# Performance work log

Hardware: AMD Instinct MI355X
Metric: run time of the kernel (lower is better)

## Reference

```python
import jax, jax.numpy as jnp
import numpy as np
from jax import lax

EPS = 1e-5
NUM_HEADS = 8


def _safe_norm(x):
    # sqrt(max(sum x^2, EPS^2)) == max(||x||, EPS); grad-safe at 0
    return jnp.sqrt(jnp.maximum(jnp.sum(x * x, axis=-1, keepdims=True), EPS * EPS))


def _project(x):
    norm = _safe_norm(x)
    max_norm = 1.0 - EPS
    scale = jnp.where(norm >= max_norm, max_norm / (norm + EPS), jnp.ones_like(norm))
    return x * scale


def _logmap0(y):
    # logarithmic_map(0, y): lambda_0 = 2/(1+EPS)
    y = _project(y)
    n = _safe_norm(y)  # clamp(min=EPS) is built in
    lam = 2.0 / (1.0 + EPS)
    return (2.0 / lam) * jnp.arctanh(n) * (y / n)


def _expmap0(v):
    # exponential_map(0, v): lambda_0 = 2/(1+EPS)
    n = _safe_norm(v)
    lam = 2.0 / (1.0 + EPS)
    return _project(jnp.tanh(lam * n / 2.0) * (v / n))


def _mobius_add(x, y):
    x = _project(x)
    y = _project(y)
    xy = jnp.sum(x * y, axis=-1, keepdims=True)
    xn = jnp.sum(x * x, axis=-1, keepdims=True)
    yn = jnp.sum(y * y, axis=-1, keepdims=True)
    num = (1.0 + 2.0 * xy + yn) * x + (1.0 - xn) * y
    den = 1.0 + 2.0 * xy + xn * yn + EPS
    return _project(num / den)


def _hyp_linear(x, W, b):
    # HyperbolicLinear.forward: project -> logmap0 -> linear -> expmap0 -> mobius-add bias
    x = _project(x)
    xt = _logmap0(x)
    t = xt @ W.T
    r = _expmap0(t)
    r = _mobius_add(r, jnp.broadcast_to(b, r.shape))
    return r


def setup_inputs() -> dict:
    key = jax.random.key(0)
    ks = jax.random.split(key, 11)
    B, S, E = 4, 512, 512

    def xavier(k, shape):
        bound = np.sqrt(6.0 / (shape[0] + shape[1]))
        return jax.random.uniform(k, shape, jnp.float32, -bound, bound)

    return {
        "query": jax.random.normal(ks[0], (B, S, E), jnp.float32),
        "key": jax.random.normal(ks[1], (B, S, E), jnp.float32),
        "value": jax.random.normal(ks[2], (B, S, E), jnp.float32),
        "Wq": xavier(ks[3], (E, E)), "bq": 0.01 * jax.random.normal(ks[4], (E,), jnp.float32),
        "Wk": xavier(ks[5], (E, E)), "bk": 0.01 * jax.random.normal(ks[6], (E,), jnp.float32),
        "Wv": xavier(ks[7], (E, E)), "bv": 0.01 * jax.random.normal(ks[8], (E,), jnp.float32),
        "Wo": xavier(ks[9], (E, E)), "bo": 0.01 * jax.random.normal(ks[10], (E,), jnp.float32),
    }


def reference(query, key, value, Wq, bq, Wk, bk, Wv, bv, Wo, bo):
    B, S, E = query.shape
    H = NUM_HEADS
    D = E // H

    Q = _hyp_linear(query, Wq, bq).reshape(B, S, H, D).transpose(0, 2, 1, 3)  # [B,H,S,D]
    K = _hyp_linear(key, Wk, bk).reshape(B, S, H, D).transpose(0, 2, 1, 3)
    V = _hyp_linear(value, Wv, bv).reshape(B, S, H, D).transpose(0, 2, 1, 3)

    # Pairwise Poincare distance: d(q,k) = acosh(1 + 2||q-k||^2/((1-|q|^2)(1-|k|^2)) + EPS)
    q = _project(Q)
    k = _project(K)
    qn = jnp.sum(q * q, axis=-1)  # [B,H,S]
    kn = jnp.sum(k * k, axis=-1)  # [B,H,S]
    qk = jnp.einsum('bhqd,bhkd->bhqk', q, k)
    num = jnp.maximum(qn[..., :, None] + kn[..., None, :] - 2.0 * qk, 0.0)
    den = jnp.maximum((1.0 - qn)[..., :, None] * (1.0 - kn)[..., None, :], EPS)
    dist = jnp.arccosh(1.0 + 2.0 * num / den + EPS)  # [B,H,Sq,Sk]
    attn = jax.nn.softmax(-dist, axis=-1)

    # Sequential Mobius-add accumulation over key/value positions
    wt = jnp.moveaxis(attn, 3, 0)  # [Sk,B,H,Sq]
    vt = jnp.moveaxis(V, 2, 0)     # [Sk,B,H,D]

    @jax.checkpoint
    def step(ws, wv):
        wj, vj = wv  # wj: [B,H,Sq], vj: [B,H,D]
        return _mobius_add(ws, wj[..., None] * vj[:, :, None, :]), None

    ws0 = jnp.zeros((B, H, S, D), query.dtype)
    attended, _ = lax.scan(step, ws0, (wt, vt))  # [B,H,Sq,D]

    attended = attended.transpose(0, 2, 1, 3).reshape(B, S, E)
    return _hyp_linear(attended, Wo, bo)
```

## Files before the change

kernel.cpp:

```cpp
#include <hip/hip_runtime.h>
#include <math.h>

#define EPS  1e-5f
#define EPS2 1e-10f
#define MAXN (1.0f - EPS)

using short8  = __attribute__((ext_vector_type(8))) short;
using floatx4 = __attribute__((ext_vector_type(4))) float;
using float2v = __attribute__((ext_vector_type(2))) float;

template <int CTRL>
static __device__ __forceinline__ float qperm(float x) {
  return __int_as_float(__builtin_amdgcn_update_dpp(
      __float_as_int(x), __float_as_int(x), CTRL, 0xF, 0xF, false));
}
#define QP_XOR1    0xB1
#define QP_XOR2    0x4E
#define QP_HALFMIR 0x141

#if __has_builtin(__builtin_elementwise_fma)
static __device__ __forceinline__ float2v fma2(float2v a, float2v b, float2v c) {
  return __builtin_elementwise_fma(a, b, c);
}
#else
static __device__ __forceinline__ float2v fma2(float2v a, float2v b, float2v c) {
  float2v r; r.x = fmaf(a.x, b.x, c.x); r.y = fmaf(a.y, b.y, c.y); return r;
}
#endif

static __device__ __forceinline__ int pack_hi2(float a, float b) {
  return (int)((__float_as_uint(a) >> 16) | (__float_as_uint(b) & 0xFFFF0000u));
}
static __device__ __forceinline__ float hi_of(float a) {
  return __uint_as_float(__float_as_uint(a) & 0xFFFF0000u);
}

static __device__ __forceinline__ float logmap_f(float ss) {
  const float r = sqrtf(fmaxf(ss, EPS2));
  float at;
  if (r >= MAXN) {
    at = 0.5f * logf((r * (2.0f - EPS) + EPS) / (EPS * (1.0f + r)));
  } else {
    at = 0.5f * logf((1.0f + r) / (1.0f - r));
  }
  return (1.0f + EPS) * at / r;
}

__global__ __launch_bounds__(256) void k_gemm_mfma(
    const float* __restrict__ A0, const float* __restrict__ A1, const float* __restrict__ A2,
    const float* __restrict__ W0, const float* __restrict__ W1, const float* __restrict__ W2,
    float* __restrict__ Cbase) {
  const int z = blockIdx.z;
  const float* A = (z == 0) ? A0 : ((z == 1) ? A1 : A2);
  const float* W = (z == 0) ? W0 : ((z == 1) ? W1 : W2);
  float* C = Cbase + (size_t)z * (2048 * 512);
  __shared__ int Ahi[64][36], Alo[64][36], Whi[64][36], Wlo[64][36];
  __shared__ float f_lds[64];
  const int t = threadIdx.x;
  const int n0 = blockIdx.x * 64;
  const int m0 = blockIdx.y * 64;
  const int row = t >> 2, c0 = (t & 3) * 16, ci = (t & 3) * 8;
  const int w = t >> 6, lane = t & 63;
  const int quad = lane >> 4, l16 = lane & 15;
  const int mw = (w & 1) * 32, nw = (w >> 1) * 32;
  floatx4 acc[2][2];
#pragma unroll
  for (int i = 0; i < 2; ++i)
#pragma unroll
    for (int j = 0; j < 2; ++j) acc[i][j] = (floatx4){0.f, 0.f, 0.f, 0.f};
  float ssq = 0.0f;

  for (int k0 = 0; k0 < 512; k0 += 64) {
    float4 av[4], wv[4];
#pragma unroll
    for (int i = 0; i < 4; ++i) {
      av[i] = *(const float4*)&A[(size_t)(n0 + row) * 512 + k0 + c0 + 4 * i];
      wv[i] = *(const float4*)&W[(size_t)(m0 + row) * 512 + k0 + c0 + 4 * i];
    }
    int pAh[8], pAl[8], pWh[8], pWl[8];
#pragma unroll
    for (int i = 0; i < 4; ++i) {
      ssq = fmaf(av[i].x, av[i].x, ssq); ssq = fmaf(av[i].y, av[i].y, ssq);
      ssq = fmaf(av[i].z, av[i].z, ssq); ssq = fmaf(av[i].w, av[i].w, ssq);
      pAh[2 * i]     = pack_hi2(av[i].x, av[i].y);
      pAh[2 * i + 1] = pack_hi2(av[i].z, av[i].w);
      pAl[2 * i]     = pack_hi2(av[i].x - hi_of(av[i].x), av[i].y - hi_of(av[i].y));
      pAl[2 * i + 1] = pack_hi2(av[i].z - hi_of(av[i].z), av[i].w - hi_of(av[i].w));
      pWh[2 * i]     = pack_hi2(wv[i].x, wv[i].y);
      pWh[2 * i + 1] = pack_hi2(wv[i].z, wv[i].w);
      pWl[2 * i]     = pack_hi2(wv[i].x - hi_of(wv[i].x), wv[i].y - hi_of(wv[i].y));
      pWl[2 * i + 1] = pack_hi2(wv[i].z - hi_of(wv[i].z), wv[i].w - hi_of(wv[i].w));
    }
    __syncthreads();
    *(int4*)&Ahi[row][ci]     = *(int4*)&pAh[0];
    *(int4*)&Ahi[row][ci + 4] = *(int4*)&pAh[4];
    *(int4*)&Alo[row][ci]     = *(int4*)&pAl[0];
    *(int4*)&Alo[row][ci + 4] = *(int4*)&pAl[4];
    *(int4*)&Whi[row][ci]     = *(int4*)&pWh[0];
    *(int4*)&Whi[row][ci + 4] = *(int4*)&pWh[4];
    *(int4*)&Wlo[row][ci]     = *(int4*)&pWl[0];
    *(int4*)&Wlo[row][ci + 4] = *(int4*)&pWl[4];
    __syncthreads();
#pragma unroll
    for (int kk = 0; kk < 64; kk += 32) {
      short8 ah[2], al[2], bh[2], bl[2];
#pragma unroll
      for (int i = 0; i < 2; ++i) {
        ah[i] = *(const short8*)&((const short*)Ahi[mw + i * 16 + l16])[kk + quad * 8];
        al[i] = *(const short8*)&((const short*)Alo[mw + i * 16 + l16])[kk + quad * 8];
        bh[i] = *(const short8*)&((const short*)Whi[nw + i * 16 + l16])[kk + quad * 8];
        bl[i] = *(const short8*)&((const short*)Wlo[nw + i * 16 + l16])[kk + quad * 8];
      }
#pragma unroll
      for (int i = 0; i < 2; ++i)
#pragma unroll
        for (int j = 0; j < 2; ++j) {
          acc[i][j] = __builtin_amdgcn_mfma_f32_16x16x32_bf16(ah[i], bh[j], acc[i][j], 0, 0, 0);
          acc[i][j] = __builtin_amdgcn_mfma_f32_16x16x32_bf16(ah[i], bl[j], acc[i][j], 0, 0, 0);
          acc[i][j] = __builtin_amdgcn_mfma_f32_16x16x32_bf16(al[i], bh[j], acc[i][j], 0, 0, 0);
        }
    }
  }
  ssq += qperm<QP_XOR1>(ssq);
  ssq += qperm<QP_XOR2>(ssq);
  if ((t & 3) == 0) f_lds[row] = logmap_f(ssq);
  __syncthreads();
#pragma unroll
  for (int i = 0; i < 2; ++i) {
    const int lrow_base = mw + i * 16 + quad * 4;
#pragma unroll
    for (int r = 0; r < 4; ++r) {
      const float fv = f_lds[lrow_base + r];
#pragma unroll
      for (int j = 0; j < 2; ++j)
        C[(size_t)(n0 + lrow_base + r) * 512 + m0 + nw + j * 16 + l16] = fv * acc[i][j][r];
    }
  }
}

__global__ __launch_bounds__(256) void k_post(const float* __restrict__ tin,
                                              const float* __restrict__ b0,
                                              const float* __restrict__ b1,
                                              const float* __restrict__ b2,
                                              float* __restrict__ o0, float* __restrict__ o1,
                                              float* __restrict__ o2,
                                              float* __restrict__ nrm0, float* __restrict__ nrm1,
                                              float* __restrict__ nrm2,
                                              float* __restrict__ rowsum_init, int final_mode) {
  const int nrow = blockIdx.x, z = blockIdx.y, t = threadIdx.x;
  const float* tv = tin + ((size_t)z * 2048 + nrow) * 512;
  const float* bias = (z == 0) ? b0 : ((z == 1) ? b1 : b2);
  const int e0 = 2 * t;
  const float2 tp = *(const float2*)&tv[e0];
  const float2 bp = *(const float2*)&bias[e0];
  float p_tt = tp.x * tp.x + tp.y * tp.y;
  float p_tb = tp.x * bp.x + tp.y * bp.y;
  float p_bb = bp.x * bp.x + bp.y * bp.y;
#pragma unroll
  for (int m = 32; m; m >>= 1) {
    p_tt += __shfl_xor(p_tt, m, 64);
    p_tb += __shfl_xor(p_tb, m, 64);
    p_bb += __shfl_xor(p_bb, m, 64);
  }
  __shared__ float red[4][3];
  const int lane = t & 63, w = t >> 6;
  if (lane == 0) { red[w][0] = p_tt; red[w][1] = p_tb; red[w][2] = p_bb; }
  __syncthreads();
  const float s_tt = red[0][0] + red[1][0] + red[2][0] + red[3][0];
  const float s_tb = red[0][1] + red[1][1] + red[2][1] + red[3][1];
  const float s_bb = red[0][2] + red[1][2] + red[2][2] + red[3][2];
  const float tn = sqrtf(fmaxf(s_tt, EPS2));
  const float th = tanhf(tn / (1.0f + EPS));
  const float g = th / tn;
  const float rnorm = th * (sqrtf(s_tt) / tn);
  const float sr = (rnorm >= MAXN) ? (MAXN / (rnorm + EPS)) : 1.0f;
  const float gr = g * sr;
  const float rn = (rnorm * sr) * (rnorm * sr);
  const float bnorm = sqrtf(fmaxf(s_bb, EPS2));
  const float sb = (bnorm >= MAXN) ? (MAXN / (bnorm + EPS)) : 1.0f;
  const float xy = gr * sb * s_tb;
  const float yn = (sb * sb) * s_bb;
  const float Af = 1.0f + 2.0f * xy + yn;
  const float Cf = 1.0f - rn;
  const float den = 1.0f + 2.0f * xy + rn * yn + EPS;
  const float id = 1.0f / den;
  const float on_raw = (Af * Af * rn + 2.0f * Af * Cf * xy + Cf * Cf * yn) * (id * id);
  const float no = sqrtf(fmaxf(on_raw, EPS2));
  const float so = (no >= MAXN) ? (MAXN / (no + EPS)) : 1.0f;
  const float ms = id * so;
  const float ca = gr * Af * ms;
  const float cb = sb * Cf * ms;
  const float v0 = ca * tp.x + cb * bp.x;
  const float v1 = ca * tp.y + cb * bp.y;
  if (final_mode) {
    float2 o; o.x = v0; o.y = v1;
    *(float2*)&o0[(size_t)nrow * 512 + e0] = o;
    return;
  }
  float hp = v0 * v0 + v1 * v1;
#pragma unroll
  for (int m = 16; m; m >>= 1) hp += __shfl_xor(hp, m, 64);
  const float hnr = sqrtf(fmaxf(hp, EPS2));
  float sh = 1.0f;
  if (z != 2) sh = (hnr >= MAXN) ? (MAXN / (hnr + EPS)) : 1.0f;
  float* outz = (z == 0) ? o0 : ((z == 1) ? o1 : o2);
  float* nz = (z == 0) ? nrm0 : ((z == 1) ? nrm1 : nrm2);
  const int b = nrow >> 9, s = nrow & 511, h = e0 >> 6, d = e0 & 63;
  float2 o; o.x = v0 * sh; o.y = v1 * sh;
  *(float2*)&outz[(((size_t)(b * 8 + h) * 512 + s) * 64 + d)] = o;
  if ((t & 31) == 0) nz[(size_t)(b * 8 + h) * 512 + s] = hp * sh * sh;
  if (z == 0 && t < 8) rowsum_init[((size_t)(nrow >> 9) * 8 + t) * 512 + (nrow & 511)] = 0.0f;
}

__global__ __launch_bounds__(256) void k_logits(const float* __restrict__ Q,
                                                const float* __restrict__ K,
                                                const float* __restrict__ qn,
                                                const float* __restrict__ kn,
                                                float* __restrict__ attn,
                                                float* __restrict__ rowsum) {
  const int bh = blockIdx.z;
  const int i0 = blockIdx.x * 64;
  const int j0 = blockIdx.y * 64;
  const float* Qb = Q + (size_t)bh * 512 * 64;
  const float* Kb = K + (size_t)bh * 512 * 64;
  __shared__ int Qhi[64][36], Qlo[64][36], Khi[64][36], Klo[64][36];
  const int t = threadIdx.x;
  const int row = t >> 2, c0 = (t & 3) * 16, ci = (t & 3) * 8;
  const int w = t >> 6, lane = t & 63;
  const int quad = lane >> 4, l16 = lane & 15;
  const int mw = (w & 1) * 32, nw = (w >> 1) * 32;
  float4 qv4[4], kv4[4];
#pragma unroll
  for (int i = 0; i < 4; ++i) {
    qv4[i] = *(const float4*)&Qb[(size_t)(i0 + row) * 64 + c0 + 4 * i];
    kv4[i] = *(const float4*)&Kb[(size_t)(j0 + row) * 64 + c0 + 4 * i];
  }
  int pQh[8], pQl[8], pKh[8], pKl[8];
#pragma unroll
  for (int i = 0; i < 4; ++i) {
    pQh[2 * i]     = pack_hi2(qv4[i].x, qv4[i].y);
    pQh[2 * i + 1] = pack_hi2(qv4[i].z, qv4[i].w);
    pQl[2 * i]     = pack_hi2(qv4[i].x - hi_of(qv4[i].x), qv4[i].y - hi_of(qv4[i].y));
    pQl[2 * i + 1] = pack_hi2(qv4[i].z - hi_of(qv4[i].z), qv4[i].w - hi_of(qv4[i].w));
    pKh[2 * i]     = pack_hi2(kv4[i].x, kv4[i].y);
    pKh[2 * i + 1] = pack_hi2(kv4[i].z, kv4[i].w);
    pKl[2 * i]     = pack_hi2(kv4[i].x - hi_of(kv4[i].x), kv4[i].y - hi_of(kv4[i].y));
    pKl[2 * i + 1] = pack_hi2(kv4[i].z - hi_of(kv4[i].z), kv4[i].w - hi_of(kv4[i].w));
  }
  *(int4*)&Qhi[row][ci]     = *(int4*)&pQh[0];
  *(int4*)&Qhi[row][ci + 4] = *(int4*)&pQh[4];
  *(int4*)&Qlo[row][ci]     = *(int4*)&pQl[0];
  *(int4*)&Qlo[row][ci + 4] = *(int4*)&pQl[4];
  *(int4*)&Khi[row][ci]     = *(int4*)&pKh[0];
  *(int4*)&Khi[row][ci + 4] = *(int4*)&pKh[4];
  *(int4*)&Klo[row][ci]     = *(int4*)&pKl[0];
  *(int4*)&Klo[row][ci + 4] = *(int4*)&pKl[4];
  __syncthreads();
  floatx4 acc[2][2];
#pragma unroll
  for (int i = 0; i < 2; ++i)
#pragma unroll
    for (int j = 0; j < 2; ++j) acc[i][j] = (floatx4){0.f, 0.f, 0.f, 0.f};
#pragma unroll
  for (int kk = 0; kk < 64; kk += 32) {
    short8 ah[2], al[2], bhv[2], blv[2];
#pragma unroll
    for (int i = 0; i < 2; ++i) {
      ah[i]  = *(const short8*)&((const short*)Qhi[mw + i * 16 + l16])[kk + quad * 8];
      al[i]  = *(const short8*)&((const short*)Qlo[mw + i * 16 + l16])[kk + quad * 8];
      bhv[i] = *(const short8*)&((const short*)Khi[nw + i * 16 + l16])[kk + quad * 8];
      blv[i] = *(const short8*)&((const short*)Klo[nw + i * 16 + l16])[kk + quad * 8];
    }
#pragma unroll
    for (int i = 0; i < 2; ++i)
#pragma unroll
      for (int j = 0; j < 2; ++j) {
        acc[i][j] = __builtin_amdgcn_mfma_f32_16x16x32_bf16(ah[i], bhv[j], acc[i][j], 0, 0, 0);
        acc[i][j] = __builtin_amdgcn_mfma_f32_16x16x32_bf16(ah[i], blv[j], acc[i][j], 0, 0, 0);
        acc[i][j] = __builtin_amdgcn_mfma_f32_16x16x32_bf16(al[i], bhv[j], acc[i][j], 0, 0, 0);
      }
  }
#pragma unroll
  for (int i = 0; i < 2; ++i) {
    float rs_acc[4] = {0.f, 0.f, 0.f, 0.f};
#pragma unroll
    for (int r = 0; r < 4; ++r) {
      const int grow = i0 + mw + i * 16 + quad * 4 + r;
      const float qni = qn[(size_t)bh * 512 + grow];
      const float rq = 1.0f - qni;
#pragma unroll
      for (int j = 0; j < 2; ++j) {
        const int gcol = j0 + nw + j * 16 + l16;
        const float knj = kn[(size_t)bh * 512 + gcol];
        const float num = fmaxf(qni + knj - 2.0f * acc[i][j][r], 0.0f);
        const float den = fmaxf(rq * (1.0f - knj), EPS);
        const float wv = fmaf(2.0f * num, __builtin_amdgcn_rcpf(den), EPS);
        const float s_ = 1.0f + wv + sqrtf(wv * (wv + 2.0f));
        const float rr = __builtin_amdgcn_rcpf(s_);
        rs_acc[r] += rr;
        attn[((size_t)bh * 512 + grow) * 512 + gcol] = rr;
      }
    }
#pragma unroll
    for (int r = 0; r < 4; ++r) {
      float v = rs_acc[r];
      v += __shfl_xor(v, 1, 64); v += __shfl_xor(v, 2, 64);
      v += __shfl_xor(v, 4, 64); v += __shfl_xor(v, 8, 64);
      if (l16 == 0)
        atomicAdd(&rowsum[(size_t)bh * 512 + i0 + mw + i * 16 + quad * 4 + r], v);
    }
  }
}

__global__ __launch_bounds__(256) void k_scan(const float* __restrict__ V,
                                              const float* __restrict__ vn,
                                              const float* __restrict__ rw,
                                              const float* __restrict__ rowsum,
                                              float* __restrict__ att) {
  __shared__ __align__(16) float v_lds[64 * 64];
  __shared__ __align__(16) float swyn_lds[64 * 66];
  const int blk = blockIdx.x;
  const int bh = blk >> 4;
  const int i0 = (blk & 15) * 32;
  const int t = threadIdx.x;
  const int lane = t & 63, w = t >> 6;
  const int row_blk = w * 8 + (lane >> 3);
  const int sub = lane & 7;
  const int d0 = sub * 8;
  const float* Vb = V + (size_t)bh * 512 * 64;
  const float* vnb = vn + (size_t)bh * 512;
  const float* arow = rw + ((size_t)bh * 512 + i0 + row_blk) * 512;
  const float inv_s = __builtin_amdgcn_rcpf(rowsum[(size_t)bh * 512 + i0 + row_blk]);

  float2v wsv[4];
#pragma unroll
  for (int k = 0; k < 4; ++k) wsv[k] = (float2v){0.f, 0.f};
  float xn = 0.0f;

  for (int jc = 0; jc < 512; jc += 64) {
#pragma unroll
    for (int it = 0; it < 4; ++it) {
      const int idx4 = it * 256 + t;
      *(float4*)&v_lds[idx4 * 4] = *(const float4*)&Vb[(size_t)jc * 64 + idx4 * 4];
    }
    const float4 a0 = *(const float4*)&arow[jc + sub * 8];
    const float4 a1 = *(const float4*)&arow[jc + sub * 8 + 4];
    const float4 n0 = *(const float4*)&vnb[jc + sub * 8];
    const float4 n1 = *(const float4*)&vnb[jc + sub * 8 + 4];
    const float wq[8] = {a0.x, a0.y, a0.z, a0.w, a1.x, a1.y, a1.z, a1.w};
    const float nq[8] = {n0.x, n0.y, n0.z, n0.w, n1.x, n1.y, n1.z, n1.w};
#pragma unroll
    for (int e = 0; e < 8; ++e) {
      const float wgt = wq[e] * inv_s;
      float2 p; p.x = wgt; p.y = (wgt * wgt) * nq[e];
      *(float2*)&swyn_lds[(sub * 8 + e) * 66 + row_blk * 2] = p;
    }
    __syncthreads();

#pragma unroll
    for (int j = 0; j < 64; ++j) {
      const float2 sy2 = *(const float2*)&swyn_lds[j * 66 + row_blk * 2];
      const float4 v0 = *(const float4*)&v_lds[j * 64 + d0];
      const float4 v1 = *(const float4*)&v_lds[j * 64 + d0 + 4];
      const float2v vv0 = {v0.x, v0.y}, vv1 = {v0.z, v0.w};
      const float2v vv2 = {v1.x, v1.y}, vv3 = {v1.z, v1.w};
      const float sw = sy2.x, yn = sy2.y;
      const float xnyn1 = fmaf(xn, yn, 1.0f + EPS);
      const float sxy   = xn + yn;
      const float ynp1  = 1.0f + yn;
      const float Cfsw  = (1.0f - xn) * sw;
      float2v da = wsv[0] * vv0;
      da = fma2(wsv[1], vv1, da);
      float2v db = wsv[2] * vv2;
      db = fma2(wsv[3], vv3, db);
      const float2v sv = da + db;
      float d = sv.x + sv.y;
      d += qperm<QP_XOR1>(d);
      d += qperm<QP_XOR2>(d);
      d += qperm<QP_HALFMIR>(d);
      const float xy  = sw * d;
      const float den = fmaf(2.0f, xy, xnyn1);
      const float s2  = fmaf(2.0f, xy, sxy);
      const float Af  = fmaf(2.0f, xy, ynp1);
      const float id  = __builtin_amdgcn_rcpf(den);
      const float dn  = den - EPS;
      const float am  = Af * id;
      const float cm  = Cfsw * id;
      xn = (s2 * id) * (dn * id);
      const float2v amv = {am, am};
      const float2v cmv = {cm, cm};
      wsv[0] = fma2(amv, wsv[0], cmv * vv0);
      wsv[1] = fma2(amv, wsv[1], cmv * vv1);
      wsv[2] = fma2(amv, wsv[2], cmv * vv2);
      wsv[3] = fma2(amv, wsv[3], cmv * vv3);
    }
    __syncthreads();
  }
  const int b = bh >> 3, h = bh & 7;
  float* o = att + (((size_t)b * 512 + i0 + row_blk) * 512 + h * 64 + d0);
  float4 s0; s0.x = wsv[0].x; s0.y = wsv[0].y; s0.z = wsv[1].x; s0.w = wsv[1].y;
  float4 s1; s1.x = wsv[2].x; s1.y = wsv[2].y; s1.z = wsv[3].x; s1.w = wsv[3].y;
  *(float4*)&o[0] = s0;
  *(float4*)&o[4] = s1;
}

extern "C" void kernel_launch(void* const* d_in, const int* in_sizes, int n_in,
                              void* d_out, int out_size, void* d_ws, size_t ws_size,
                              hipStream_t stream) {
  const float* query = (const float*)d_in[0];
  const float* key_  = (const float*)d_in[1];
  const float* value = (const float*)d_in[2];
  const float* Wq = (const float*)d_in[3];
  const float* bq = (const float*)d_in[4];
  const float* Wk = (const float*)d_in[5];
  const float* bk = (const float*)d_in[6];
  const float* Wv = (const float*)d_in[7];
  const float* bv = (const float*)d_in[8];
  const float* Wo = (const float*)d_in[9];
  const float* bo = (const float*)d_in[10];
  float* ws = (float*)d_ws;
  const size_t M = 1u << 20;
  float* Qb     = ws;
  float* Kb     = ws + 1 * M;
  float* Vb     = ws + 2 * M;
  float* qn     = ws + 3 * M;
  float* kn     = qn + 16384;
  float* vn     = kn + 16384;
  float* rowsum = vn + 16384;
  float* rw     = ws + 4 * M;
  float* t3     = ws + 12 * M;
  float* att    = ws + 15 * M;
  float* to_    = ws + 16 * M;

  k_gemm_mfma<<<dim3(32, 8, 3), 256, 0, stream>>>(query, key_, value, Wq, Wk, Wv, t3);
  k_post<<<dim3(2048, 3), 256, 0, stream>>>(t3, bq, bk, bv, Qb, Kb, Vb, qn, kn, vn,
                                            rowsum, 0);
  k_logits<<<dim3(8, 8, 32), 256, 0, stream>>>(Qb, Kb, qn, kn, rw, rowsum);
  k_scan<<<512, 256, 0, stream>>>(Vb, vn, rw, rowsum, att);
  k_gemm_mfma<<<dim3(32, 8, 1), 256, 0, stream>>>(att, att, att, Wo, Wo, Wo, to_);
  k_post<<<dim3(2048, 1), 256, 0, stream>>>(to_, bo, bo, bo, (float*)d_out,
                                            nullptr, nullptr, nullptr, nullptr, nullptr,
                                            nullptr, 1);
}
```

Before: 229.9 us.

## Split scan rows across 16 lanes with 4 dims each, doubling grid

The sequential Mobius-add scan kernel now gives each query row to 16 lanes holding 4 head dimensions each, instead of 8 lanes holding 8. Each block covers 16 rows, and the grid doubles to 1024 blocks. This shortens the per-lane serial dependency chain and raises the number of waves to hide latency on the sequential recurrence. In exchange it adds one more DPP reduction step per iteration, and each block reloads the V tile for half as many rows, doubling V traffic into LDS.

```diff
diff --git a/kernel.cpp b/kernel.cpp
--- a/kernel.cpp
+++ b/kernel.cpp
@@ -17,6 +17,7 @@
 #define QP_XOR1    0xB1
 #define QP_XOR2    0x4E
 #define QP_HALFMIR 0x141
+#define QP_MIRROR  0x140
 
 #if __has_builtin(__builtin_elementwise_fma)
 static __device__ __forceinline__ float2v fma2(float2v a, float2v b, float2v c) {
@@ -318,23 +319,20 @@
                                               const float* __restrict__ rowsum,
                                               float* __restrict__ att) {
   __shared__ __align__(16) float v_lds[64 * 64];
-  __shared__ __align__(16) float swyn_lds[64 * 66];
+  __shared__ __align__(16) float swyn_lds[64 * 34];
   const int blk = blockIdx.x;
-  const int bh = blk >> 4;
-  const int i0 = (blk & 15) * 32;
+  const int bh = blk >> 5;
+  const int i0 = (blk & 31) * 16;
   const int t = threadIdx.x;
-  const int lane = t & 63, w = t >> 6;
-  const int row_blk = w * 8 + (lane >> 3);
-  const int sub = lane & 7;
-  const int d0 = sub * 8;
+  const int row_blk = t >> 4;
+  const int sub = t & 15;
+  const int d0 = sub * 4;
   const float* Vb = V + (size_t)bh * 512 * 64;
   const float* vnb = vn + (size_t)bh * 512;
   const float* arow = rw + ((size_t)bh * 512 + i0 + row_blk) * 512;
   const float inv_s = __builtin_amdgcn_rcpf(rowsum[(size_t)bh * 512 + i0 + row_blk]);
 
-  float2v wsv[4];
-#pragma unroll
-  for (int k = 0; k < 4; ++k) wsv[k] = (float2v){0.f, 0.f};
+  float2v ws0 = {0.f, 0.f}, ws1 = {0.f, 0.f};
   float xn = 0.0f;
 
   for (int jc = 0; jc < 512; jc += 64) {
@@ -343,41 +341,35 @@
       const int idx4 = it * 256 + t;
       *(float4*)&v_lds[idx4 * 4] = *(const float4*)&Vb[(size_t)jc * 64 + idx4 * 4];
     }
-    const float4 a0 = *(const float4*)&arow[jc + sub * 8];
-    const float4 a1 = *(const float4*)&arow[jc + sub * 8 + 4];
-    const float4 n0 = *(const float4*)&vnb[jc + sub * 8];
-    const float4 n1 = *(const float4*)&vnb[jc + sub * 8 + 4];
-    const float wq[8] = {a0.x, a0.y, a0.z, a0.w, a1.x, a1.y, a1.z, a1.w};
-    const float nq[8] = {n0.x, n0.y, n0.z, n0.w, n1.x, n1.y, n1.z, n1.w};
-#pragma unroll
-    for (int e = 0; e < 8; ++e) {
+    const float4 aw = *(const float4*)&arow[jc + sub * 4];
+    const float4 nv = *(const float4*)&vnb[jc + sub * 4];
+    const float wq[4] = {aw.x, aw.y, aw.z, aw.w};
+    const float nq[4] = {nv.x, nv.y, nv.z, nv.w};
+#pragma unroll
+    for (int e = 0; e < 4; ++e) {
       const float wgt = wq[e] * inv_s;
       float2 p; p.x = wgt; p.y = (wgt * wgt) * nq[e];
-      *(float2*)&swyn_lds[(sub * 8 + e) * 66 + row_blk * 2] = p;
+      *(float2*)&swyn_lds[(sub * 4 + e) * 34 + row_blk * 2] = p;
     }
     __syncthreads();
 
 #pragma unroll
     for (int j = 0; j < 64; ++j) {
-      const float2 sy2 = *(const float2*)&swyn_lds[j * 66 + row_blk * 2];
-      const float4 v0 = *(const float4*)&v_lds[j * 64 + d0];
-      const float4 v1 = *(const float4*)&v_lds[j * 64 + d0 + 4];
-      const float2v vv0 = {v0.x, v0.y}, vv1 = {v0.z, v0.w};
-      const float2v vv2 = {v1.x, v1.y}, vv3 = {v1.z, v1.w};
+      const float2 sy2 = *(const float2*)&swyn_lds[j * 34 + row_blk * 2];
+      const float4 v4 = *(const float4*)&v_lds[j * 64 + d0];
+      const float2v vv0 = {v4.x, v4.y}, vv1 = {v4.z, v4.w};
       const float sw = sy2.x, yn = sy2.y;
       const float xnyn1 = fmaf(xn, yn, 1.0f + EPS);
       const float sxy   = xn + yn;
       const float ynp1  = 1.0f + yn;
       const float Cfsw  = (1.0f - xn) * sw;
-      float2v da = wsv[0] * vv0;
-      da = fma2(wsv[1], vv1, da);
-      float2v db = wsv[2] * vv2;
-      db = fma2(wsv[3], vv3, db);
-      const float2v sv = da + db;
-      float d = sv.x + sv.y;
+      float2v da = ws0 * vv0;
+      da = fma2(ws1, vv1, da);
+      float d = da.x + da.y;
       d += qperm<QP_XOR1>(d);
       d += qperm<QP_XOR2>(d);
       d += qperm<QP_HALFMIR>(d);
+      d += qperm<QP_MIRROR>(d);
       const float xy  = sw * d;
       const float den = fmaf(2.0f, xy, xnyn1);
       const float s2  = fmaf(2.0f, xy, sxy);
@@ -389,19 +381,15 @@
       xn = (s2 * id) * (dn * id);
       const float2v amv = {am, am};
       const float2v cmv = {cm, cm};
-      wsv[0] = fma2(amv, wsv[0], cmv * vv0);
-      wsv[1] = fma2(amv, wsv[1], cmv * vv1);
-      wsv[2] = fma2(amv, wsv[2], cmv * vv2);
-      wsv[3] = fma2(amv, wsv[3], cmv * vv3);
+      ws0 = fma2(amv, ws0, cmv * vv0);
+      ws1 = fma2(amv, ws1, cmv * vv1);
     }
     __syncthreads();
   }
   const int b = bh >> 3, h = bh & 7;
   float* o = att + (((size_t)b * 512 + i0 + row_blk) * 512 + h * 64 + d0);
-  float4 s0; s0.x = wsv[0].x; s0.y = wsv[0].y; s0.z = wsv[1].x; s0.w = wsv[1].y;
-  float4 s1; s1.x = wsv[2].x; s1.y = wsv[2].y; s1.z = wsv[3].x; s1.w = wsv[3].y;
+  float4 s0; s0.x = ws0.x; s0.y = ws0.y; s0.z = ws1.x; s0.w = ws1.y;
   *(float4*)&o[0] = s0;
-  *(float4*)&o[4] = s1;
 }
 
 extern "C" void kernel_launch(void* const* d_in, const int* in_sizes, int n_in,
@@ -436,7 +424,7 @@
   k_post<<<dim3(2048, 3), 256, 0, stream>>>(t3, bq, bk, bv, Qb, Kb, Vb, qn, kn, vn,
                                             rowsum, 0);
   k_logits<<<dim3(8, 8, 32), 256, 0, stream>>>(Qb, Kb, qn, kn, rw, rowsum);
-  k_scan<<<512, 256, 0, stream>>>(Vb, vn, rw, rowsum, att);
+  k_scan<<<1024, 256, 0, stream>>>(Vb, vn, rw, rowsum, att);
   k_gemm_mfma<<<dim3(32, 8, 1), 256, 0, stream>>>(att, att, att, Wo, Wo, Wo, to_);
   k_post<<<dim3(2048, 1), 256, 0, stream>>>(to_, bo, bo, bo, (float*)d_out,
                                             nullptr, nullptr, nullptr, nullptr, nullptr,
```

New measurement: 271.0 us. 17.9% more time.

## Break scan dependency chain by precomputing next-step dot via Gram terms

Applied to the files above, without the earlier changes.

Restructures the sequential Mobius-add scan so the dot product of the accumulator with the next value vector is computed one step ahead. It uses the linear update identity <ws',v_{j+1}> = am*<ws,v_{j+1}> + cm*<v_j,v_{j+1}>, with the adjacent-row Gram terms precomputed per chunk into shared memory. This takes the cross-lane reduction off the serial critical path so it can overlap with the scalar update math. It adds an extra reduction per chunk, a new LDS array and a barrier, and changes the floating-point ordering of the dot product.

```diff
diff --git a/kernel.cpp b/kernel.cpp
--- a/kernel.cpp
+++ b/kernel.cpp
@@ -319,6 +319,7 @@
                                               float* __restrict__ att) {
   __shared__ __align__(16) float v_lds[64 * 64];
   __shared__ __align__(16) float swyn_lds[64 * 66];
+  __shared__ float g_lds[64];
   const int blk = blockIdx.x;
   const int bh = blk >> 4;
   const int i0 = (blk & 15) * 32;
@@ -357,28 +358,60 @@
     }
     __syncthreads();
 
+    {
+      const int jg = row_blk * 2;
+      const float4 va0 = *(const float4*)&v_lds[jg * 64 + d0];
+      const float4 va1 = *(const float4*)&v_lds[jg * 64 + d0 + 4];
+      const float4 vb0 = *(const float4*)&v_lds[(jg + 1) * 64 + d0];
+      const float4 vb1 = *(const float4*)&v_lds[(jg + 1) * 64 + d0 + 4];
+      const float4 vc0 = *(const float4*)&v_lds[((jg + 2) & 63) * 64 + d0];
+      const float4 vc1 = *(const float4*)&v_lds[((jg + 2) & 63) * 64 + d0 + 4];
+      float p0 = va0.x * vb0.x + va0.y * vb0.y + va0.z * vb0.z + va0.w * vb0.w +
+                 va1.x * vb1.x + va1.y * vb1.y + va1.z * vb1.z + va1.w * vb1.w;
+      float p1 = vb0.x * vc0.x + vb0.y * vc0.y + vb0.z * vc0.z + vb0.w * vc0.w +
+                 vb1.x * vc1.x + vb1.y * vc1.y + vb1.z * vc1.z + vb1.w * vc1.w;
+      p0 += qperm<QP_XOR1>(p0); p0 += qperm<QP_XOR2>(p0); p0 += qperm<QP_HALFMIR>(p0);
+      p1 += qperm<QP_XOR1>(p1); p1 += qperm<QP_XOR2>(p1); p1 += qperm<QP_HALFMIR>(p1);
+      if (sub == 0) { g_lds[jg] = p0; g_lds[jg + 1] = p1; }
+    }
+    float2v vcur[4];
+    {
+      const float4 c0v = *(const float4*)&v_lds[d0];
+      const float4 c1v = *(const float4*)&v_lds[d0 + 4];
+      vcur[0] = (float2v){c0v.x, c0v.y}; vcur[1] = (float2v){c0v.z, c0v.w};
+      vcur[2] = (float2v){c1v.x, c1v.y}; vcur[3] = (float2v){c1v.z, c1v.w};
+    }
+    float2v dd = wsv[0] * vcur[0];
+    dd = fma2(wsv[1], vcur[1], dd);
+    dd = fma2(wsv[2], vcur[2], dd);
+    dd = fma2(wsv[3], vcur[3], dd);
+    float D = dd.x + dd.y;
+    D += qperm<QP_XOR1>(D); D += qperm<QP_XOR2>(D); D += qperm<QP_HALFMIR>(D);
+    __syncthreads();
+
 #pragma unroll
     for (int j = 0; j < 64; ++j) {
       const float2 sy2 = *(const float2*)&swyn_lds[j * 66 + row_blk * 2];
-      const float4 v0 = *(const float4*)&v_lds[j * 64 + d0];
-      const float4 v1 = *(const float4*)&v_lds[j * 64 + d0 + 4];
-      const float2v vv0 = {v0.x, v0.y}, vv1 = {v0.z, v0.w};
-      const float2v vv2 = {v1.x, v1.y}, vv3 = {v1.z, v1.w};
       const float sw = sy2.x, yn = sy2.y;
       const float xnyn1 = fmaf(xn, yn, 1.0f + EPS);
       const float sxy   = xn + yn;
       const float ynp1  = 1.0f + yn;
       const float Cfsw  = (1.0f - xn) * sw;
-      float2v da = wsv[0] * vv0;
-      da = fma2(wsv[1], vv1, da);
-      float2v db = wsv[2] * vv2;
-      db = fma2(wsv[3], vv3, db);
-      const float2v sv = da + db;
-      float d = sv.x + sv.y;
-      d += qperm<QP_XOR1>(d);
-      d += qperm<QP_XOR2>(d);
-      d += qperm<QP_HALFMIR>(d);
-      const float xy  = sw * d;
+      float2v vnx[4];
+      float E = 0.0f;
+      if (j < 63) {
+        const float4 nx0 = *(const float4*)&v_lds[(j + 1) * 64 + d0];
+        const float4 nx1 = *(const float4*)&v_lds[(j + 1) * 64 + d0 + 4];
+        vnx[0] = (float2v){nx0.x, nx0.y}; vnx[1] = (float2v){nx0.z, nx0.w};
+        vnx[2] = (float2v){nx1.x, nx1.y}; vnx[3] = (float2v){nx1.z, nx1.w};
+        float2v ee = wsv[0] * vnx[0];
+        ee = fma2(wsv[1], vnx[1], ee);
+        ee = fma2(wsv[2], vnx[2], ee);
+        ee = fma2(wsv[3], vnx[3], ee);
+        E = ee.x + ee.y;
+        E += qperm<QP_XOR1>(E); E += qperm<QP_XOR2>(E); E += qperm<QP_HALFMIR>(E);
+      }
+      const float xy  = sw * D;
       const float den = fmaf(2.0f, xy, xnyn1);
       const float s2  = fmaf(2.0f, xy, sxy);
       const float Af  = fmaf(2.0f, xy, ynp1);
@@ -389,10 +422,14 @@
       xn = (s2 * id) * (dn * id);
       const float2v amv = {am, am};
       const float2v cmv = {cm, cm};
-      wsv[0] = fma2(amv, wsv[0], cmv * vv0);
-      wsv[1] = fma2(amv, wsv[1], cmv * vv1);
-      wsv[2] = fma2(amv, wsv[2], cmv * vv2);
-      wsv[3] = fma2(amv, wsv[3], cmv * vv3);
+      wsv[0] = fma2(amv, wsv[0], cmv * vcur[0]);
+      wsv[1] = fma2(amv, wsv[1], cmv * vcur[1]);
+      wsv[2] = fma2(amv, wsv[2], cmv * vcur[2]);
+      wsv[3] = fma2(amv, wsv[3], cmv * vcur[3]);
+      if (j < 63) {
+        D = fmaf(am, E, cm * g_lds[j]);
+        vcur[0] = vnx[0]; vcur[1] = vnx[1]; vcur[2] = vnx[2]; vcur[3] = vnx[3];
+      }
     }
     __syncthreads();
   }
```

Measured after the change: 239.9 us. 1.04x slower.
